# Kernel tuning notes

Measured on AMD Instinct MI355X. Metric: run time of the kernel, lower is better.

## Reference

```python
import jax, jax.numpy as jnp
import numpy as np

MAX_SET_SIZE = 32  # f1_query_max_set_size


def setup_inputs() -> dict:
    key = jax.random.key(0)
    k1, k2, k3, k4 = jax.random.split(key, 4)
    B, Lq, L, d_qk, d_v = 8, 512, 4096, 64, 64
    q = jax.random.normal(k1, (B, Lq, d_qk), dtype=jnp.float32)
    k = jax.random.normal(k2, (B, L, d_qk), dtype=jnp.float32)
    v = jax.random.normal(k3, (B, L, d_v), dtype=jnp.float32)
    mask = jax.random.randint(k4, (B * Lq, L), 0, 2).astype(bool)
    return {"q": q, "k": k, "v": v, "mask": mask}


def _query_conditioned_subset_pool(rank_scores, v, batch_idx, mask, max_set_size):
    # rank_scores/mask: [N, L]; v: [B, L, d_v]
    N, L = rank_scores.shape
    keep = min(max_set_size, L)
    neg_inf = jnp.finfo(rank_scores.dtype).min
    masked_scores = jnp.where(mask, rank_scores.astype(jnp.float32), neg_inf)
    _, top_idx = jax.lax.top_k(masked_scores, keep)          # [N, keep]
    picked = jnp.take_along_axis(mask, top_idx, axis=1)
    sortable = jnp.where(picked, top_idx, L)                 # sentinel L for unpicked
    sortable = jnp.sort(sortable, axis=1)                    # restore index order
    picked = sortable < L
    safe_idx = jnp.where(picked, sortable, 0)                # [N, keep]
    sel_v = v[batch_idx[:, None], safe_idx]                  # [N, keep, d_v]
    sel_scores = jnp.take_along_axis(rank_scores, safe_idx, axis=1)
    sel_scores = jnp.where(picked, sel_scores, neg_inf)
    attn = jax.nn.softmax(sel_scores, axis=1)
    non_empty = picked.any(axis=1, keepdims=True)
    attn = jnp.where(picked & non_empty, attn, jnp.zeros_like(attn))
    return jnp.einsum('nk,nkd->nd', attn.astype(sel_v.dtype), sel_v)


def reference(q, k, v, mask):
    B, Lq, d_qk = q.shape
    L = k.shape[1]
    d_v = v.shape[-1]
    scale = 1.0 / float(np.sqrt(d_qk))
    # rank_scores [B, Lq, L] -> flat chains [B*Lq, L]
    rank_scores = jnp.einsum('bqd,bld->bql', q, k) * scale
    rs_flat = rank_scores.reshape(B * Lq, L)
    batch_idx = jnp.repeat(jnp.arange(B), Lq)
    # f1 = mean over masked support: sum_v / clamp(count, 1)
    mask_f = mask.astype(q.dtype)                            # [B*Lq, L]
    count = jnp.clip(mask_f.sum(axis=1), 1.0, None)          # [B*Lq]
    sum_v = jnp.einsum('bql,bld->bqd', mask_f.reshape(B, Lq, L), v).reshape(B * Lq, d_v)
    mean_out = sum_v / count[:, None]
    # f1_query_mode='add': query-conditioned restricted pooling over top-k subset
    q_ctx = _query_conditioned_subset_pool(rs_flat, v, batch_idx, mask, MAX_SET_SIZE)
    out = mean_out + q_ctx
    return out.reshape(B, Lq, d_v)
```

## Files before the change

kernel.cpp:

```cpp
#include <hip/hip_runtime.h>
#include <float.h>
#include <math.h>

#define LQ   512
#define LL   4096
#define DD   64
#define KEEP 32
#define NB   8
#define NROWS (NB * LQ)

#define RT    32
#define NLC   8
#define LC    (LL / NLC)
#define LSP   128
#define NPAIR (LC / LSP)

#define WS_VT    (NROWS * LL)
#define WS_TOTAL (WS_VT + (NB * DD * LL) / 2)

#define MASKED_KEY 0x00800000u

typedef short  bf16x8 __attribute__((ext_vector_type(8)));
typedef float  f32x4  __attribute__((ext_vector_type(4)));

__device__ __forceinline__ float dot4(float4 a, float4 b) {
    return a.x * b.x + a.y * b.y + a.z * b.z + a.w * b.w;
}
__device__ __forceinline__ unsigned short f2bf(float f) {
    unsigned int u = __float_as_uint(f);
    return (unsigned short)((u + 0x7FFFu + ((u >> 16) & 1u)) >> 16);
}

#define TP_LB 256
__global__ __launch_bounds__(256) void k_vt(
    const float* __restrict__ v, unsigned short* __restrict__ vt)
{
    __shared__ unsigned short tile[DD][TP_LB + 8];
    const int t  = threadIdx.x;
    const int b  = blockIdx.x >> 4;
    const int l0 = (blockIdx.x & 15) * TP_LB;

    const float4* vg = reinterpret_cast<const float4*>(v + ((size_t)b * LL + l0) * DD);
    #pragma unroll
    for (int i = 0; i < 16; ++i) {
        int j = t + 256 * i;
        float4 f = vg[j];
        int l = j >> 4, dq = (j & 15) * 4;
        tile[dq + 0][l] = f2bf(f.x);
        tile[dq + 1][l] = f2bf(f.y);
        tile[dq + 2][l] = f2bf(f.z);
        tile[dq + 3][l] = f2bf(f.w);
    }
    __syncthreads();
    const int d = t >> 2, seg = t & 3;
    const uint4* src = reinterpret_cast<const uint4*>(&tile[d][seg * 64]);
    uint4* dst = reinterpret_cast<uint4*>(vt + ((size_t)b * DD + d) * LL + l0 + seg * 64);
    #pragma unroll
    for (int i = 0; i < 8; ++i) dst[i] = src[i];
}

__global__ __launch_bounds__(256) void k_mean(
    const int* __restrict__ mask,
    const unsigned short* __restrict__ vt,
    float* __restrict__ out)
{
    __shared__ float sums[4][4][16][16];
    __shared__ float cnt_s[4][16];

    const int t     = threadIdx.x;
    const int wave  = t >> 6;
    const int lane  = t & 63;
    const int n0    = blockIdx.x * 16;
    const int b     = n0 / LQ;
    const int row_a = lane & 15;
    const int chunk = lane >> 4;

    const int* mrow = mask + (size_t)(n0 + row_a) * LL + wave * 1024 + chunk * 8;
    const unsigned short* vbase = vt + (size_t)b * DD * LL + wave * 1024 + chunk * 8;

    f32x4 acc[4];
    #pragma unroll
    for (int dt = 0; dt < 4; ++dt) acc[dt] = (f32x4){0.f, 0.f, 0.f, 0.f};
    int cnt = 0;

    for (int l0 = 0; l0 < 1024; l0 += 32) {
        int4 ma = *reinterpret_cast<const int4*>(mrow + l0);
        int4 mb = *reinterpret_cast<const int4*>(mrow + l0 + 4);
        cnt += (ma.x != 0) + (ma.y != 0) + (ma.z != 0) + (ma.w != 0)
             + (mb.x != 0) + (mb.y != 0) + (mb.z != 0) + (mb.w != 0);
        unsigned int p[4];
        p[0] = (ma.x ? 0x3F80u : 0u) | (ma.y ? 0x3F800000u : 0u);
        p[1] = (ma.z ? 0x3F80u : 0u) | (ma.w ? 0x3F800000u : 0u);
        p[2] = (mb.x ? 0x3F80u : 0u) | (mb.y ? 0x3F800000u : 0u);
        p[3] = (mb.z ? 0x3F80u : 0u) | (mb.w ? 0x3F800000u : 0u);
        bf16x8 afrag = *reinterpret_cast<bf16x8*>(p);
        #pragma unroll
        for (int dt = 0; dt < 4; ++dt) {
            bf16x8 bfrag = *reinterpret_cast<const bf16x8*>(
                vbase + (size_t)(dt * 16 + row_a) * LL + l0);
            acc[dt] = __builtin_amdgcn_mfma_f32_16x16x32_bf16(afrag, bfrag, acc[dt], 0, 0, 0);
        }
    }
    cnt += __shfl_xor(cnt, 16);
    cnt += __shfl_xor(cnt, 32);
    if (lane < 16) cnt_s[wave][lane] = (float)cnt;
    #pragma unroll
    for (int dt = 0; dt < 4; ++dt)
        #pragma unroll
        for (int r = 0; r < 4; ++r)
            sums[wave][dt][chunk * 4 + r][row_a] = acc[dt][r];
    __syncthreads();

    const int d = t & 63, rgrp = t >> 6;
    #pragma unroll
    for (int rr = 0; rr < 4; ++rr) {
        const int row = rgrp * 4 + rr;
        float s = sums[0][d >> 4][row][d & 15] + sums[1][d >> 4][row][d & 15]
                + sums[2][d >> 4][row][d & 15] + sums[3][d >> 4][row][d & 15];
        float c = cnt_s[0][row] + cnt_s[1][row] + cnt_s[2][row] + cnt_s[3][row];
        if (c < 1.f) c = 1.f;
        out[(size_t)(n0 + row) * DD + d] = s / c;
    }
}

__global__ __launch_bounds__(256)
__attribute__((amdgpu_waves_per_eu(2, 4)))
void k_scores(
    const float* __restrict__ q,
    const float* __restrict__ kmat,
    const int*   __restrict__ mask,
    float*       __restrict__ ws_sc)
{
    __shared__ float4 Ss4[16 * LSP];

    const int t    = threadIdx.x;
    const int wave = t >> 6;
    const int lane = t & 63;
    const int rt   = blockIdx.x >> 3;
    const int lc   = blockIdx.x & (NLC - 1);
    const int n0   = rt * RT;
    const int b    = n0 / LQ;
    const int lbase = lc * LC;

    int qbase[8];
    #pragma unroll
    for (int p = 0; p < 8; ++p)
        qbase[p] = __builtin_amdgcn_readfirstlane((n0 + wave * 8 + p) * DD);

    const float4* kg = reinterpret_cast<const float4*>(kmat) + (size_t)b * LL * 16;

    for (int s = 0; s < NPAIR; ++s) {
        const int l0 = lbase + s * LSP;
        __syncthreads();
        #pragma unroll
        for (int i = 0; i < 2; ++i)
            #pragma unroll
            for (int j = 0; j < 4; ++j)
                Ss4[(wave * 4 + j) * LSP + lane + 64 * i] =
                    kg[(size_t)(l0 + lane + 64 * i) * 16 + wave * 4 + j];
        __syncthreads();

        float acc0[8], acc1[8];
        #pragma unroll
        for (int p = 0; p < 8; ++p) { acc0[p] = 0.f; acc1[p] = 0.f; }
        #pragma unroll
        for (int dc = 0; dc < 16; ++dc) {
            float4 ka = Ss4[dc * LSP + lane];
            float4 kb = Ss4[dc * LSP + 64 + lane];
            #pragma unroll
            for (int p = 0; p < 8; ++p) {
                float4 q4 = *reinterpret_cast<const float4*>(q + qbase[p] + dc * 4);
                acc0[p] += dot4(ka, q4);
                acc1[p] += dot4(kb, q4);
            }
        }
        #pragma unroll
        for (int p = 0; p < 8; ++p) {
            const int r = wave * 8 + p;
            int m0 = mask[(size_t)(n0 + r) * LL + l0 + lane];
            int m1 = mask[(size_t)(n0 + r) * LL + l0 + 64 + lane];
            ws_sc[(size_t)(n0 + r) * LL + l0 + lane]      = m0 ? acc0[p] * 0.125f : -FLT_MAX;
            ws_sc[(size_t)(n0 + r) * LL + l0 + 64 + lane] = m1 ? acc1[p] * 0.125f : -FLT_MAX;
        }
    }
}

__global__ __launch_bounds__(256, 3) void k_select(
    const float* __restrict__ vmat,
    const float* __restrict__ ws,
    float*       __restrict__ out)
{
    __shared__ unsigned int selKey[4][KEEP];
    __shared__ int          selIdx[4][KEEP];
    __shared__ float        wsel[4][KEEP];
    __shared__ int          selCnt[4], eqCnt[4];

    const int t    = threadIdx.x;
    const int wave = t >> 6;
    const int lane = t & 63;
    const int row  = blockIdx.x * 4 + wave;
    const int b    = row / LQ;

    float o = out[(size_t)row * DD + lane];

    unsigned int key[64];
    {
        const float4* sg = reinterpret_cast<const float4*>(ws) + (size_t)row * (LL / 4);
        #pragma unroll
        for (int i = 0; i < 16; ++i) {
            float4 f = sg[lane + 64 * i];
            float vals[4] = { f.x, f.y, f.z, f.w };
            #pragma unroll
            for (int c = 0; c < 4; ++c) {
                unsigned int u = __float_as_uint(vals[c]);
                key[4 * i + c] = ((int)u < 0) ? ~u : (u | 0x80000000u);
            }
        }
    }

    unsigned int T = 0u;
    for (int bit = 31; bit >= 0; --bit) {
        const unsigned int cand = T | (1u << bit);
        int cnt = 0;
        #pragma unroll
        for (int e = 0; e < 64; ++e)
            cnt += (int)__popcll(__ballot(key[e] >= cand));
        if (cnt >= KEEP) T = cand;
    }
    int cgt = 0;
    #pragma unroll
    for (int e = 0; e < 64; ++e)
        cgt += (int)__popcll(__ballot(key[e] > T));
    const unsigned int quota = (unsigned int)(KEEP - cgt);
    const bool take_eq = (T != MASKED_KEY);

    if (lane < KEEP) { wsel[wave][lane] = 0.f; selIdx[wave][lane] = 0; }
    if (lane == 0)   { selCnt[wave] = 0; eqCnt[wave] = 0; }
    __asm__ volatile("s_waitcnt lgkmcnt(0)" ::: "memory");
    #pragma unroll
    for (int e = 0; e < 64; ++e) {
        unsigned int k = key[e];
        if (k > T) {
            int slot = atomicAdd(&selCnt[wave], 1);
            selKey[wave][slot] = k;
            selIdx[wave][slot] = 256 * (e >> 2) + 4 * lane + (e & 3);
        } else if (take_eq && k == T) {
            int t2 = atomicAdd(&eqCnt[wave], 1);
            if (t2 < (int)quota) {
                int slot = atomicAdd(&selCnt[wave], 1);
                selKey[wave][slot] = k;
                selIdx[wave][slot] = 256 * (e >> 2) + 4 * lane + (e & 3);
            }
        }
    }
    __asm__ volatile("s_waitcnt lgkmcnt(0)" ::: "memory");
    const int S = selCnt[wave];

    if (S > 0) {
        float vj = -FLT_MAX;
        if (lane < S) {
            unsigned int kk = selKey[wave][lane];
            unsigned int u = (kk & 0x80000000u) ? (kk ^ 0x80000000u) : ~kk;
            vj = __uint_as_float(u);
        }
        float mx = vj;
        #pragma unroll
        for (int off = 1; off < 64; off <<= 1) mx = fmaxf(mx, __shfl_xor(mx, off));
        float e = (lane < S) ? expf(vj - mx) : 0.f;
        float sum = e;
        #pragma unroll
        for (int off = 1; off < 64; off <<= 1) sum += __shfl_xor(sum, off);
        if (lane < S) wsel[wave][lane] = e / sum;
        __asm__ volatile("s_waitcnt lgkmcnt(0)" ::: "memory");
        const float* vb = vmat + (size_t)b * LL * DD + lane;
        #pragma unroll
        for (int j = 0; j < KEEP; ++j) {
            float wj = wsel[wave][j];
            int   ij = selIdx[wave][j];
            o += wj * vb[(size_t)ij * DD];
        }
    }
    out[(size_t)row * DD + lane] = o;
}

#define QT   2
#define NT   256
#define NTILES (LL / NT)

__global__ __launch_bounds__(NT, 4) void ga_fused_fb(
    const float* __restrict__ q, const float* __restrict__ kmat,
    const float* __restrict__ vmat, const int* __restrict__ mask,
    float* __restrict__ out)
{
    __shared__ float sc[QT][LL];
    __shared__ float q_s[QT][DD];
    __shared__ unsigned long long mbits[QT][LL / 64];
    __shared__ float redv[4][QT][DD];
    __shared__ float mean_s[QT][DD];
    __shared__ int   count_s[QT];
    __shared__ int   sel_idx[QT][KEEP];
    __shared__ float sel_val[QT][KEEP];
    __shared__ int   sel_cnt[QT];
    __shared__ float wred[4];
    __shared__ int   ired[4];
    __shared__ int   brk;
    __shared__ float wgt[QT][KEEP];

    const int t = threadIdx.x, wave = t >> 6, lane = t & 63;
    const int n0 = blockIdx.x * QT, b = n0 / LQ;

    if (t < QT) sel_cnt[t] = 0;
    if (t < QT * DD) q_s[t >> 6][t & 63] = q[(size_t)(n0 + (t >> 6)) * DD + (t & 63)];
    __syncthreads();

    const float4* q4_0 = reinterpret_cast<const float4*>(&q_s[0][0]);
    const float4* q4_1 = reinterpret_cast<const float4*>(&q_s[1][0]);
    for (int tile = 0; tile < NTILES; ++tile) {
        int l = tile * NT + t;
        const float4* kr = reinterpret_cast<const float4*>(kmat + (size_t)(b * LL + l) * DD);
        float d0 = 0.f, d1 = 0.f;
        #pragma unroll
        for (int i = 0; i < 16; ++i) {
            float4 kk = kr[i], qa = q4_0[i], qb = q4_1[i];
            d0 += kk.x * qa.x + kk.y * qa.y + kk.z * qa.z + kk.w * qa.w;
            d1 += kk.x * qb.x + kk.y * qb.y + kk.z * qb.z + kk.w * qb.w;
        }
        int mv0 = mask[(size_t)n0 * LL + l];
        int mv1 = mask[(size_t)(n0 + 1) * LL + l];
        unsigned long long b0 = __ballot(mv0 != 0);
        unsigned long long b1 = __ballot(mv1 != 0);
        if (lane == 0) { mbits[0][tile * 4 + wave] = b0; mbits[1][tile * 4 + wave] = b1; }
        sc[0][l] = mv0 ? d0 * 0.125f : -FLT_MAX;
        sc[1][l] = mv1 ? d1 * 0.125f : -FLT_MAX;
    }
    __syncthreads();

    if (wave < QT) {
        int c = (int)__popcll(mbits[wave][lane]);
        for (int off = 32; off >= 1; off >>= 1) c += __shfl_down(c, off);
        if (lane == 0) count_s[wave] = c;
    }
    {
        float acc0 = 0.f, acc1 = 0.f;
        const int g = wave, d = lane;
        for (int wi = 0; wi < LL / 64; ++wi) {
            unsigned long long w0 = mbits[0][wi], w1 = mbits[1][wi];
            const float* vp = vmat + (size_t)(b * LL + wi * 64 + g) * DD + d;
            #pragma unroll 4
            for (int ii = 0; ii < 16; ++ii) {
                int sh = g + 4 * ii;
                float vv = vp[(size_t)(4 * ii) * DD];
                if ((w0 >> sh) & 1ULL) acc0 += vv;
                if ((w1 >> sh) & 1ULL) acc1 += vv;
            }
        }
        redv[g][0][d] = acc0; redv[g][1][d] = acc1;
    }
    __syncthreads();
    if (t < QT * DD) {
        int qt = t >> 6, dd = t & 63;
        float s2 = redv[0][qt][dd] + redv[1][qt][dd] + redv[2][qt][dd] + redv[3][qt][dd];
        int c = count_s[qt]; if (c < 1) c = 1;
        mean_s[qt][dd] = s2 / (float)c;
    }
    __syncthreads();

    for (int qt = 0; qt < QT; ++qt) {
        for (int s = 0; s < KEEP; ++s) {
            float m = -FLT_MAX; int mi = LL;
            for (int j = 0; j < NTILES; ++j) {
                int l = j * NT + t;
                float val = sc[qt][l];
                if (val > m) { m = val; mi = l; }
            }
            for (int off = 32; off >= 1; off >>= 1) {
                float ov = __shfl_down(m, off);
                int   oi = __shfl_down(mi, off);
                if (ov > m || (ov == m && oi < mi)) { m = ov; mi = oi; }
            }
            if (lane == 0) { wred[wave] = m; ired[wave] = mi; }
            __syncthreads();
            if (t == 0) {
                float bv = wred[0]; int bi = ired[0];
                for (int w2 = 1; w2 < 4; ++w2) {
                    float ov = wred[w2]; int oi = ired[w2];
                    if (ov > bv || (ov == bv && oi < bi)) { bv = ov; bi = oi; }
                }
                if (bv > -FLT_MAX) {
                    sel_idx[qt][s] = bi; sel_val[qt][s] = bv; sel_cnt[qt] = s + 1;
                    sc[qt][bi] = -FLT_MAX; brk = 0;
                } else brk = 1;
            }
            __syncthreads();
            if (brk) break;
        }
    }

    if (wave < QT) {
        int qt = wave, S = sel_cnt[qt];
        if (S > 0) {
            float mx = sel_val[qt][0];
            float e = 0.f;
            if (lane < S) e = expf(sel_val[qt][lane] - mx);
            float ssum = e;
            for (int off = 32; off >= 1; off >>= 1) ssum += __shfl_xor(ssum, off);
            if (lane < S) wgt[qt][lane] = e / ssum;
        }
    }
    __syncthreads();
    if (wave < QT) {
        int qt = wave, S = sel_cnt[qt];
        float o = mean_s[qt][lane];
        for (int j = 0; j < S; ++j)
            o += wgt[qt][j] * vmat[(size_t)(b * LL + sel_idx[qt][j]) * DD + lane];
        out[(size_t)(n0 + qt) * DD + lane] = o;
    }
}

extern "C" void kernel_launch(void* const* d_in, const int* in_sizes, int n_in,
                              void* d_out, int out_size, void* d_ws, size_t ws_size,
                              hipStream_t stream) {
    const float* q    = (const float*)d_in[0];
    const float* kmat = (const float*)d_in[1];
    const float* vmat = (const float*)d_in[2];
    const int*   mask = (const int*)d_in[3];
    float* out = (float*)d_out;

    const size_t need = (size_t)WS_TOTAL * sizeof(float);
    if (ws_size >= need) {
        float* ws = (float*)d_ws;
        unsigned short* vt = (unsigned short*)(ws + WS_VT);
        hipLaunchKernelGGL(k_scores, dim3((NROWS / RT) * NLC), dim3(256), 0, stream,
                           q, kmat, mask, ws);
        hipLaunchKernelGGL(k_vt, dim3(NB * 16), dim3(256), 0, stream, vmat, vt);
        hipLaunchKernelGGL(k_mean, dim3(NROWS / 16), dim3(256), 0, stream,
                           mask, vt, out);
        hipLaunchKernelGGL(k_select, dim3(NROWS / 4), dim3(256), 0, stream,
                           vmat, ws, out);
    } else {
        hipLaunchKernelGGL(ga_fused_fb, dim3(NROWS / QT), dim3(NT), 0, stream,
                           q, kmat, vmat, mask, out);
    }
}
```

Baseline: 304.2 us.

## Do per-chunk top-k inside score kernel, pass only candidates to select

The score kernel no longer writes the full masked score matrix to workspace. Each block runs a radix-style threshold search over its 512-column chunk and emits only the 32 best candidate keys and indices per row. The select kernel then does the final top-32 over 256 candidates per row instead of 4096 scores. This removes a large global write and read of the score matrix, at the cost of extra ballot-based selection work and register pressure in the score kernel.

After: 303.3 us. About the same (-0.3%).

```diff
diff --git a/kernel.cpp b/kernel.cpp
--- a/kernel.cpp
+++ b/kernel.cpp
@@ -15,7 +15,8 @@
 #define LSP   128
 #define NPAIR (LC / LSP)
 
-#define WS_VT    (NROWS * LL)
+#define WS_CI    (NROWS * NLC * KEEP)
+#define WS_VT    (2 * NROWS * NLC * KEEP)
 #define WS_TOTAL (WS_VT + (NB * DD * LL) / 2)
 
 #define MASKED_KEY 0x00800000u
@@ -29,6 +30,10 @@
 __device__ __forceinline__ unsigned short f2bf(float f) {
     unsigned int u = __float_as_uint(f);
     return (unsigned short)((u + 0x7FFFu + ((u >> 16) & 1u)) >> 16);
+}
+__device__ __forceinline__ unsigned int f2key(float f) {
+    unsigned int u = __float_as_uint(f);
+    return ((int)u < 0) ? ~u : (u | 0x80000000u);
 }
 
 #define TP_LB 256
@@ -129,7 +134,8 @@
     const float* __restrict__ q,
     const float* __restrict__ kmat,
     const int*   __restrict__ mask,
-    float*       __restrict__ ws_sc)
+    unsigned int* __restrict__ ck,
+    int*          __restrict__ ci)
 {
     __shared__ float4 Ss4[16 * LSP];
 
@@ -149,6 +155,9 @@
 
     const float4* kg = reinterpret_cast<const float4*>(kmat) + (size_t)b * LL * 16;
 
+    unsigned int key[8][2 * NPAIR];
+
+    #pragma unroll
     for (int s = 0; s < NPAIR; ++s) {
         const int l0 = lbase + s * LSP;
         __syncthreads();
@@ -179,15 +188,62 @@
             const int r = wave * 8 + p;
             int m0 = mask[(size_t)(n0 + r) * LL + l0 + lane];
             int m1 = mask[(size_t)(n0 + r) * LL + l0 + 64 + lane];
-            ws_sc[(size_t)(n0 + r) * LL + l0 + lane]      = m0 ? acc0[p] * 0.125f : -FLT_MAX;
-            ws_sc[(size_t)(n0 + r) * LL + l0 + 64 + lane] = m1 ? acc1[p] * 0.125f : -FLT_MAX;
-        }
-    }
-}
-
-__global__ __launch_bounds__(256, 3) void k_select(
+            key[p][2 * s]     = m0 ? f2key(acc0[p] * 0.125f) : MASKED_KEY;
+            key[p][2 * s + 1] = m1 ? f2key(acc1[p] * 0.125f) : MASKED_KEY;
+        }
+    }
+
+    const unsigned long long lmask =
+        (lane == 63) ? 0x7fffffffffffffffull : ((1ull << lane) - 1ull);
+    #pragma unroll
+    for (int p = 0; p < 8; ++p) {
+        const int row = n0 + wave * 8 + p;
+        unsigned int T = 0u;
+        for (int bit = 31; bit >= 0; --bit) {
+            const unsigned int cand = T | (1u << bit);
+            int cnt = 0;
+            #pragma unroll
+            for (int e = 0; e < 2 * NPAIR; ++e)
+                cnt += (int)__popcll(__ballot(key[p][e] >= cand));
+            if (cnt >= KEEP) T = cand;
+        }
+        const bool take_eq = (T != MASKED_KEY);
+        unsigned int* ckr = ck + ((size_t)row * NLC + lc) * KEEP;
+        int*          cir = ci + ((size_t)row * NLC + lc) * KEEP;
+        int nsel = 0;
+        #pragma unroll
+        for (int e = 0; e < 2 * NPAIR; ++e) {
+            unsigned long long bg = __ballot(key[p][e] > T);
+            int pre = (int)__popcll(bg & lmask);
+            if (key[p][e] > T) {
+                ckr[nsel + pre] = key[p][e];
+                cir[nsel + pre] = lbase + ((e >> 1) << 7) + ((e & 1) << 6) + lane;
+            }
+            nsel += (int)__popcll(bg);
+        }
+        if (take_eq) {
+            int rem = KEEP - nsel;
+            #pragma unroll
+            for (int e = 0; e < 2 * NPAIR; ++e) {
+                if (rem <= 0) break;
+                unsigned long long be = __ballot(key[p][e] == T);
+                int pre = (int)__popcll(be & lmask);
+                if (key[p][e] == T && pre < rem) {
+                    ckr[nsel + pre] = T;
+                    cir[nsel + pre] = lbase + ((e >> 1) << 7) + ((e & 1) << 6) + lane;
+                }
+                int c = (int)__popcll(be); if (c > rem) c = rem;
+                nsel += c; rem -= c;
+            }
+        }
+        if (lane >= nsel && lane < KEEP) { ckr[lane] = MASKED_KEY; cir[lane] = 0; }
+    }
+}
+
+__global__ __launch_bounds__(256) void k_select(
     const float* __restrict__ vmat,
-    const float* __restrict__ ws,
+    const unsigned int* __restrict__ ck,
+    const int* __restrict__ ci,
     float*       __restrict__ out)
 {
     __shared__ unsigned int selKey[4][KEEP];
@@ -203,33 +259,23 @@
 
     float o = out[(size_t)row * DD + lane];
 
-    unsigned int key[64];
-    {
-        const float4* sg = reinterpret_cast<const float4*>(ws) + (size_t)row * (LL / 4);
-        #pragma unroll
-        for (int i = 0; i < 16; ++i) {
-            float4 f = sg[lane + 64 * i];
-            float vals[4] = { f.x, f.y, f.z, f.w };
-            #pragma unroll
-            for (int c = 0; c < 4; ++c) {
-                unsigned int u = __float_as_uint(vals[c]);
-                key[4 * i + c] = ((int)u < 0) ? ~u : (u | 0x80000000u);
-            }
-        }
-    }
+    uint4 kk = reinterpret_cast<const uint4*>(ck + (size_t)row * (NLC * KEEP))[lane];
+    int4  ii = reinterpret_cast<const int4*>(ci + (size_t)row * (NLC * KEEP))[lane];
+    unsigned int key[4] = { kk.x, kk.y, kk.z, kk.w };
+    int          idx[4] = { ii.x, ii.y, ii.z, ii.w };
 
     unsigned int T = 0u;
     for (int bit = 31; bit >= 0; --bit) {
         const unsigned int cand = T | (1u << bit);
         int cnt = 0;
         #pragma unroll
-        for (int e = 0; e < 64; ++e)
+        for (int e = 0; e < 4; ++e)
             cnt += (int)__popcll(__ballot(key[e] >= cand));
         if (cnt >= KEEP) T = cand;
     }
     int cgt = 0;
     #pragma unroll
-    for (int e = 0; e < 64; ++e)
+    for (int e = 0; e < 4; ++e)
         cgt += (int)__popcll(__ballot(key[e] > T));
     const unsigned int quota = (unsigned int)(KEEP - cgt);
     const bool take_eq = (T != MASKED_KEY);
@@ -238,18 +284,18 @@
     if (lane == 0)   { selCnt[wave] = 0; eqCnt[wave] = 0; }
     __asm__ volatile("s_waitcnt lgkmcnt(0)" ::: "memory");
     #pragma unroll
-    for (int e = 0; e < 64; ++e) {
+    for (int e = 0; e < 4; ++e) {
         unsigned int k = key[e];
         if (k > T) {
             int slot = atomicAdd(&selCnt[wave], 1);
             selKey[wave][slot] = k;
-            selIdx[wave][slot] = 256 * (e >> 2) + 4 * lane + (e & 3);
+            selIdx[wave][slot] = idx[e];
         } else if (take_eq && k == T) {
             int t2 = atomicAdd(&eqCnt[wave], 1);
             if (t2 < (int)quota) {
                 int slot = atomicAdd(&selCnt[wave], 1);
                 selKey[wave][slot] = k;
-                selIdx[wave][slot] = 256 * (e >> 2) + 4 * lane + (e & 3);
+                selIdx[wave][slot] = idx[e];
             }
         }
     }
@@ -259,8 +305,8 @@
     if (S > 0) {
         float vj = -FLT_MAX;
         if (lane < S) {
-            unsigned int kk = selKey[wave][lane];
-            unsigned int u = (kk & 0x80000000u) ? (kk ^ 0x80000000u) : ~kk;
+            unsigned int kk2 = selKey[wave][lane];
+            unsigned int u = (kk2 & 0x80000000u) ? (kk2 ^ 0x80000000u) : ~kk2;
             vj = __uint_as_float(u);
         }
         float mx = vj;
@@ -429,14 +475,16 @@
     const size_t need = (size_t)WS_TOTAL * sizeof(float);
     if (ws_size >= need) {
         float* ws = (float*)d_ws;
+        unsigned int* ck = (unsigned int*)ws;
+        int*          ci = (int*)(ws + WS_CI);
         unsigned short* vt = (unsigned short*)(ws + WS_VT);
         hipLaunchKernelGGL(k_scores, dim3((NROWS / RT) * NLC), dim3(256), 0, stream,
-                           q, kmat, mask, ws);
+                           q, kmat, mask, ck, ci);
         hipLaunchKernelGGL(k_vt, dim3(NB * 16), dim3(256), 0, stream, vmat, vt);
         hipLaunchKernelGGL(k_mean, dim3(NROWS / 16), dim3(256), 0, stream,
                            mask, vt, out);
         hipLaunchKernelGGL(k_select, dim3(NROWS / 4), dim3(256), 0, stream,
-                           vmat, ws, out);
+                           vmat, ck, ci, out);
     } else {
         hipLaunchKernelGGL(ga_fused_fb, dim3(NROWS / QT), dim3(NT), 0, stream,
                            q, kmat, vmat, mask, out);
```

## Pack mask into ballot bitmasks in k_mean and use per-lane counts in radix select

Applied to the files above, without the earlier changes.

k_mean now runs 512 threads (8 waves over 512-column slices). It first loads the int mask with coalesced reads and compresses it via ballot into 32-bit words in shared memory, then builds the bf16 MFMA A-fragments from those bits instead of strided int4 loads. The radix-select threshold search in k_select replaces the 64 ballot/popcount pairs per bit with per-lane scalar counts followed by a shuffle-xor reduction, and drops the occupancy hint of 3 blocks from its launch bounds. This costs an extra barrier and shared-memory staging in k_mean, and can change register allocation and occupancy in k_select.

Result: slower. 334.5 us (+9.9%).

```diff
diff --git a/kernel.cpp b/kernel.cpp
--- a/kernel.cpp
+++ b/kernel.cpp
@@ -29,6 +29,10 @@
 __device__ __forceinline__ unsigned short f2bf(float f) {
     unsigned int u = __float_as_uint(f);
     return (unsigned short)((u + 0x7FFFu + ((u >> 16) & 1u)) >> 16);
+}
+__device__ __forceinline__ unsigned int f2key(float f) {
+    unsigned int u = __float_as_uint(f);
+    return ((int)u < 0) ? ~u : (u | 0x80000000u);
 }
 
 #define TP_LB 256
@@ -59,13 +63,14 @@
     for (int i = 0; i < 8; ++i) dst[i] = src[i];
 }
 
-__global__ __launch_bounds__(256) void k_mean(
+__global__ __launch_bounds__(512) void k_mean(
     const int* __restrict__ mask,
     const unsigned short* __restrict__ vt,
     float* __restrict__ out)
 {
-    __shared__ float sums[4][4][16][16];
-    __shared__ float cnt_s[4][16];
+    __shared__ unsigned int mb32[8][16][17];
+    __shared__ float sums[8][4][16][16];
+    __shared__ float cnt_s[8][16];
 
     const int t     = threadIdx.x;
     const int wave  = t >> 6;
@@ -74,26 +79,38 @@
     const int b     = n0 / LQ;
     const int row_a = lane & 15;
     const int chunk = lane >> 4;
-
-    const int* mrow = mask + (size_t)(n0 + row_a) * LL + wave * 1024 + chunk * 8;
-    const unsigned short* vbase = vt + (size_t)b * DD * LL + wave * 1024 + chunk * 8;
+    const int lbase = wave * 512;
+
+    for (int r = 0; r < 16; ++r) {
+        const int* mrow = mask + (size_t)(n0 + r) * LL + lbase;
+        #pragma unroll
+        for (int i = 0; i < 8; ++i) {
+            unsigned long long bl = __ballot(mrow[i * 64 + lane] != 0);
+            if (lane == 0) mb32[wave][r][2 * i]     = (unsigned int)bl;
+            if (lane == 1) mb32[wave][r][2 * i + 1] = (unsigned int)(bl >> 32);
+        }
+    }
+    __syncthreads();
+
+    const unsigned short* vbase = vt + (size_t)b * DD * LL + lbase + chunk * 8;
 
     f32x4 acc[4];
     #pragma unroll
     for (int dt = 0; dt < 4; ++dt) acc[dt] = (f32x4){0.f, 0.f, 0.f, 0.f};
     int cnt = 0;
 
-    for (int l0 = 0; l0 < 1024; l0 += 32) {
-        int4 ma = *reinterpret_cast<const int4*>(mrow + l0);
-        int4 mb = *reinterpret_cast<const int4*>(mrow + l0 + 4);
-        cnt += (ma.x != 0) + (ma.y != 0) + (ma.z != 0) + (ma.w != 0)
-             + (mb.x != 0) + (mb.y != 0) + (mb.z != 0) + (mb.w != 0);
+    #pragma unroll
+    for (int it = 0; it < 16; ++it) {
+        const unsigned int wbits = mb32[wave][row_a][it];
+        const unsigned int byte  = (wbits >> (chunk * 8)) & 0xFFu;
+        cnt += __popc(byte);
         unsigned int p[4];
-        p[0] = (ma.x ? 0x3F80u : 0u) | (ma.y ? 0x3F800000u : 0u);
-        p[1] = (ma.z ? 0x3F80u : 0u) | (ma.w ? 0x3F800000u : 0u);
-        p[2] = (mb.x ? 0x3F80u : 0u) | (mb.y ? 0x3F800000u : 0u);
-        p[3] = (mb.z ? 0x3F80u : 0u) | (mb.w ? 0x3F800000u : 0u);
+        p[0] = ((byte & 1u)   ? 0x3F80u : 0u) | ((byte & 2u)   ? 0x3F800000u : 0u);
+        p[1] = ((byte & 4u)   ? 0x3F80u : 0u) | ((byte & 8u)   ? 0x3F800000u : 0u);
+        p[2] = ((byte & 16u)  ? 0x3F80u : 0u) | ((byte & 32u)  ? 0x3F800000u : 0u);
+        p[3] = ((byte & 64u)  ? 0x3F80u : 0u) | ((byte & 128u) ? 0x3F800000u : 0u);
         bf16x8 afrag = *reinterpret_cast<bf16x8*>(p);
+        const int l0 = it * 32;
         #pragma unroll
         for (int dt = 0; dt < 4; ++dt) {
             bf16x8 bfrag = *reinterpret_cast<const bf16x8*>(
@@ -113,11 +130,14 @@
 
     const int d = t & 63, rgrp = t >> 6;
     #pragma unroll
-    for (int rr = 0; rr < 4; ++rr) {
-        const int row = rgrp * 4 + rr;
-        float s = sums[0][d >> 4][row][d & 15] + sums[1][d >> 4][row][d & 15]
-                + sums[2][d >> 4][row][d & 15] + sums[3][d >> 4][row][d & 15];
-        float c = cnt_s[0][row] + cnt_s[1][row] + cnt_s[2][row] + cnt_s[3][row];
+    for (int rr = 0; rr < 2; ++rr) {
+        const int row = rgrp * 2 + rr;
+        float s = 0.f, c = 0.f;
+        #pragma unroll
+        for (int w = 0; w < 8; ++w) {
+            s += sums[w][d >> 4][row][d & 15];
+            c += cnt_s[w][row];
+        }
         if (c < 1.f) c = 1.f;
         out[(size_t)(n0 + row) * DD + d] = s / c;
     }
@@ -185,7 +205,7 @@
     }
 }
 
-__global__ __launch_bounds__(256, 3) void k_select(
+__global__ __launch_bounds__(256) void k_select(
     const float* __restrict__ vmat,
     const float* __restrict__ ws,
     float*       __restrict__ out)
@@ -209,28 +229,28 @@
         #pragma unroll
         for (int i = 0; i < 16; ++i) {
             float4 f = sg[lane + 64 * i];
-            float vals[4] = { f.x, f.y, f.z, f.w };
-            #pragma unroll
-            for (int c = 0; c < 4; ++c) {
-                unsigned int u = __float_as_uint(vals[c]);
-                key[4 * i + c] = ((int)u < 0) ? ~u : (u | 0x80000000u);
-            }
+            key[4 * i + 0] = f2key(f.x);
+            key[4 * i + 1] = f2key(f.y);
+            key[4 * i + 2] = f2key(f.z);
+            key[4 * i + 3] = f2key(f.w);
         }
     }
 
     unsigned int T = 0u;
     for (int bit = 31; bit >= 0; --bit) {
         const unsigned int cand = T | (1u << bit);
-        int cnt = 0;
-        #pragma unroll
-        for (int e = 0; e < 64; ++e)
-            cnt += (int)__popcll(__ballot(key[e] >= cand));
-        if (cnt >= KEEP) T = cand;
+        int c = 0;
+        #pragma unroll
+        for (int e = 0; e < 64; ++e) c += (key[e] >= cand) ? 1 : 0;
+        #pragma unroll
+        for (int off = 1; off < 64; off <<= 1) c += __shfl_xor(c, off);
+        if (c >= KEEP) T = cand;
     }
     int cgt = 0;
     #pragma unroll
-    for (int e = 0; e < 64; ++e)
-        cgt += (int)__popcll(__ballot(key[e] > T));
+    for (int e = 0; e < 64; ++e) cgt += (key[e] > T) ? 1 : 0;
+    #pragma unroll
+    for (int off = 1; off < 64; off <<= 1) cgt += __shfl_xor(cgt, off);
     const unsigned int quota = (unsigned int)(KEEP - cgt);
     const bool take_eq = (T != MASKED_KEY);
 
@@ -433,7 +453,7 @@
         hipLaunchKernelGGL(k_scores, dim3((NROWS / RT) * NLC), dim3(256), 0, stream,
                            q, kmat, mask, ws);
         hipLaunchKernelGGL(k_vt, dim3(NB * 16), dim3(256), 0, stream, vmat, vt);
-        hipLaunchKernelGGL(k_mean, dim3(NROWS / 16), dim3(256), 0, stream,
+        hipLaunchKernelGGL(k_mean, dim3(NROWS / 16), dim3(512), 0, stream,
                            mask, vt, out);
         hipLaunchKernelGGL(k_select, dim3(NROWS / 4), dim3(256), 0, stream,
                            vmat, ws, out);
```
